# Performance work log

Measured on AMD Instinct MI355X. Metric: run time of the kernel, lower is better.

## Reference

```python
import jax, jax.numpy as jnp
import numpy as np

TEMP = 0.1
COEFF = 0.5
WARMUP = 0
S = 32 * 32  # hardcoded in the torch module


def _l2n(x, axis):
    # matches F.normalize(p=2, eps=1e-12)
    n = jnp.linalg.norm(x, axis=axis, keepdims=True)
    return x / jnp.maximum(n, 1e-12)


def _ce_first_class(pos, neg):
    # cross-entropy with label 0 on logits = [pos | neg] / T
    logits = jnp.concatenate([pos, neg], axis=1) / TEMP
    return jnp.mean(jax.nn.logsumexp(logits, axis=1) - logits[:, 0])


def _dense_losses(q_of, q_x, k_of, k_x, k_avg_dense):
    # q_of,k_of: (B,d,S) normalized; q_x,k_x: (B,C,S) normalized; k_avg_dense: (B,C) UN-normalized (torch bug preserved)
    B, C, _ = q_x.shape
    sim = jnp.einsum('bds,bdt->bst', q_of, k_of)          # (B,S,S)
    ind = jnp.argmax(sim, axis=2)                          # (B,S)
    idxg = jnp.take_along_axis(k_x, jnp.broadcast_to(ind[:, None, :], k_x.shape), axis=2)
    idxg = jax.lax.stop_gradient(idxg)                     # computed under torch.no_grad
    l_pos = jnp.sum(q_x * idxg, axis=1).reshape(-1, 1)     # (B*S,1)
    qf = jnp.transpose(q_x, (0, 2, 1)).reshape(-1, C)      # (B*S,C)
    l_neg_full = qf @ k_avg_dense.T                        # (B*S,B)
    # static mask: row n excludes column n // S
    base = np.stack([np.delete(np.arange(B), i) for i in range(B)])  # (B,B-1)
    neg_cols = jnp.asarray(np.repeat(base, S, axis=0))     # (B*S,B-1)
    l_neg = jnp.take_along_axis(l_neg_full, neg_cols, axis=1)
    return l_pos, l_neg


def _forward(original_features_q, avgpooled_global_q, x_q, avgpooled_dense_q,
             original_features_k, avgpooled_global_k, x_k, avgpooled_dense_k, epoch):
    of = jnp.concatenate([original_features_q, original_features_k], axis=0)
    ag = jnp.concatenate([avgpooled_global_q, avgpooled_global_k], axis=0)
    x = jnp.concatenate([x_q, x_k], axis=0)
    ad = jnp.concatenate([avgpooled_dense_q, avgpooled_dense_k], axis=0)

    # global InfoNCE
    agn = _l2n(ag, 1)
    sim = agn @ agn.T                                      # (2B,2B)
    n2 = sim.shape[0]
    B = n2 // 2
    rows = np.arange(n2)
    pos_cols = (rows + B) % n2
    pos = sim[jnp.asarray(rows), jnp.asarray(pos_cols)][:, None]
    neg_cols = np.stack([np.setdiff1d(rows, [i, pos_cols[i]]) for i in range(n2)])  # (2B,2B-2)
    neg = jnp.take_along_axis(sim, jnp.asarray(neg_cols), axis=1)
    global_loss = _ce_first_class(pos, neg)

    # dense InfoNCE
    b, d, h, w = of.shape
    of = _l2n(of.reshape(b, d, h * w), 1)
    xn = _l2n(x, 1)
    q_of, k_of = of[:b // 2], of[b // 2:]
    q_x, k_x = xn[:b // 2], xn[b // 2:]
    q_ad, k_ad = ad[:b // 2], ad[b // 2:]  # NOTE: un-normalized, matching the torch code
    p1, n1 = _dense_losses(q_of, q_x, k_of, k_x, k_ad)
    p2, n2_ = _dense_losses(k_of, k_x, q_of, q_x, q_ad)
    dense_loss = _ce_first_class(jnp.concatenate([p1, p2], axis=0),
                                 jnp.concatenate([n1, n2_], axis=0))

    if epoch > WARMUP:
        return COEFF * global_loss + (1.0 - COEFF) * dense_loss
    return global_loss


def setup_inputs() -> dict:
    key = jax.random.key(0)
    ks = jax.random.split(key, 8)
    B, d, C, h, w = 64, 256, 128, 32, 32
    return {
        'original_features_q': jax.random.normal(ks[0], (B, d, h, w), jnp.float32),
        'avgpooled_global_q': jax.random.normal(ks[1], (B, C), jnp.float32),
        'x_q': jax.random.normal(ks[2], (B, C, h * w), jnp.float32),
        'avgpooled_dense_q': jax.random.normal(ks[3], (B, C), jnp.float32),
        'original_features_k': jax.random.normal(ks[4], (B, d, h, w), jnp.float32),
        'avgpooled_global_k': jax.random.normal(ks[5], (B, C), jnp.float32),
        'x_k': jax.random.normal(ks[6], (B, C, h * w), jnp.float32),
        'avgpooled_dense_k': jax.random.normal(ks[7], (B, C), jnp.float32),
        'epoch': 5,
    }


def reference(original_features_q, avgpooled_global_q, x_q, avgpooled_dense_q,
              original_features_k, avgpooled_global_k, x_k, avgpooled_dense_k, epoch):
    return _forward(original_features_q, avgpooled_global_q, x_q, avgpooled_dense_q,
                    original_features_k, avgpooled_global_k, x_k, avgpooled_dense_k, epoch)
```

## Files before the change

### kernel.cpp

```cpp
#include <hip/hip_runtime.h>
#include <math.h>

#define TEMP_INV 10.0f

typedef unsigned long long u64;
typedef __attribute__((ext_vector_type(8))) __bf16 bf16x8;
typedef __attribute__((ext_vector_type(4))) float f32x4;

__device__ inline unsigned fkey(float v) {
  unsigned u = __float_as_uint(v);
  return (u & 0x80000000u) ? ~u : (u | 0x80000000u);
}

__device__ __forceinline__ void async_copy16(const void* gp, void* lp) {
  __builtin_amdgcn_global_load_lds(
      (__attribute__((address_space(1))) void*)(unsigned long long)gp,
      (__attribute__((address_space(3))) void*)(unsigned long long)lp,
      16, 0, 0);
}

__global__ __launch_bounds__(256) void kpre(
    const float* __restrict__ ofq, const float* __restrict__ ofk,
    __bf16* __restrict__ ofT, float* __restrict__ of_invn,
    const float* __restrict__ xq, const float* __restrict__ xk,
    float* __restrict__ x_invn,
    const float* __restrict__ adq, const float* __restrict__ adk,
    float* __restrict__ adt,
    const float* __restrict__ agq, const float* __restrict__ agk,
    float* __restrict__ gsum) {
  unsigned bx = blockIdx.x;
  int t = threadIdx.x;
  if (bx < 4096) {
    int s0 = (bx & 31) * 32, b = bx >> 5;
    const float* src = (b < 64) ? (ofq + (size_t)b * 262144) : (ofk + (size_t)(b - 64) * 262144);
    __shared__ __bf16 T[32][36];
    __shared__ float R[8][32];
    int dd = t >> 5, ss = t & 31;
    int wr = t >> 3, wd = t & 7;
    float ssq = 0.f;
    __bf16* out = ofT + (size_t)b * 262144 + (size_t)s0 * 256;
    for (int d0 = 0; d0 < 256; d0 += 32) {
      float v[4];
#pragma unroll
      for (int it = 0; it < 4; ++it) {
        int d = d0 + dd + 8 * it;
        v[it] = src[(size_t)d * 1024 + s0 + ss];
        ssq += v[it] * v[it];
      }
      __syncthreads();
#pragma unroll
      for (int it = 0; it < 4; ++it) T[ss][dd + 8 * it] = (__bf16)v[it];
      __syncthreads();
      *(uint2*)(out + (size_t)wr * 256 + d0 + wd * 4) = *(const uint2*)(&T[wr][wd * 4]);
    }
    R[dd][ss] = ssq;
    __syncthreads();
    if (t < 32) {
      float a = 0.f;
#pragma unroll
      for (int r = 0; r < 8; ++r) a += R[r][t];
      of_invn[b * 1024 + s0 + t] = 1.0f / fmaxf(sqrtf(a), 1e-12f);
    }
  } else if (bx < 4672) {
    unsigned px = bx - 4096;
    if (px < 512) {
      int idx = px * 256 + t;
      int b = idx >> 10, s = idx & 1023;
      const float* src = (b < 64) ? (xq + (size_t)b * 131072) : (xk + (size_t)(b - 64) * 131072);
      float acc = 0.f;
#pragma unroll 8
      for (int c = 0; c < 128; ++c) { float v = src[c * 1024 + s]; acc += v * v; }
      x_invn[idx] = 1.0f / fmaxf(sqrtf(acc), 1e-12f);
    } else {
      int i = (px - 512) * 256 + t;
      int dir = i >> 13, r = i & 8191;
      int j = r >> 7, c = r & 127;
      const float* ad = dir == 0 ? adk : adq;
      adt[dir * 8192 + c * 64 + j] = ad[j * 128 + c];
    }
  } else {
    __shared__ float logits[2][128];
    __shared__ float rinv[128];
    int ii = t >> 7, j = t & 127;
    int i = (int)(bx - 4672) * 2 + ii;
    const float* rowi = (i < 64) ? (agq + i * 128) : (agk + (i - 64) * 128);
    const float* rowj = (j < 64) ? (agq + j * 128) : (agk + (j - 64) * 128);
    float dot = 0.f, nj = 0.f;
#pragma unroll 8
    for (int c = 0; c < 128; ++c) { float a = rowi[c], bb = rowj[c]; dot += a * bb; nj += bb * bb; }
    if (ii == 0) rinv[j] = 1.0f / fmaxf(sqrtf(nj), 1e-12f);
    __syncthreads();
    logits[ii][j] = dot * rinv[i] * rinv[j] * TEMP_INV;
    __syncthreads();
    if (j == 0) {
      int pos = (i + 64) & 127;
      float m = -INFINITY;
      for (int tt = 0; tt < 128; ++tt) if (tt != i) m = fmaxf(m, logits[ii][tt]);
      float e = 0.f;
      for (int tt = 0; tt < 128; ++tt) if (tt != i) e += __expf(logits[ii][tt] - m);
      atomicAdd(gsum, m + __logf(e) - logits[ii][pos]);
    }
  }
}

__global__ __launch_bounds__(512, 2) void ksim(
    const __bf16* __restrict__ ofT, const float* __restrict__ of_invn,
    u64* __restrict__ best_row, u64* __restrict__ best_col) {
  unsigned h = blockIdx.x + (blockIdx.y << 2) + (blockIdx.z << 4);
  int xcd = h & 7;
  unsigned slot = h >> 3;
  int b = xcd + 8 * (int)(slot >> 4);
  int tile = slot & 15;
  int s0 = (tile & 3) * 256, t0 = (tile >> 2) * 256;

  const __bf16* Ag = ofT + (size_t)b * 262144;
  const __bf16* Bg = ofT + (size_t)(b + 64) * 262144;
  __shared__ __bf16 As[2][16384];
  __shared__ __bf16 Bs[2][16384];

  int t = threadIdx.x;
  int lane = t & 63, w = t >> 6;
  int lc = lane & 15, q = lane >> 4;
  int wm = w >> 2, wn = w & 3;

  f32x4 acc[8][4];
#pragma unroll
  for (int i = 0; i < 8; ++i)
#pragma unroll
    for (int j = 0; j < 4; ++j) acc[i][j] = (f32x4)(0.f);

  int aoff[8], boff[4];
#pragma unroll
  for (int i = 0; i < 8; ++i) {
    int mr = wm * 128 + i * 16 + lc;
    aoff[i] = mr * 64 + ((q ^ (mr & 7)) << 3);
  }
#pragma unroll
  for (int j = 0; j < 4; ++j) {
    int nc = wn * 64 + j * 16 + lc;
    boff[j] = nc * 64 + ((q ^ (nc & 7)) << 3);
  }

  int ms = t >> 3, gphys = t & 7;
  int lg = gphys ^ (ms & 7);
  size_t aSrc = (size_t)(s0 + ms) * 256 + lg * 8;
  size_t bSrc = (size_t)(t0 + ms) * 256 + lg * 8;

  auto STAGE = [&](int bufn, int k0) {
    char* aL = (char*)&As[bufn][0] + t * 16;
    char* bL = (char*)&Bs[bufn][0] + t * 16;
#pragma unroll
    for (int c = 0; c < 4; ++c) {
      async_copy16(Ag + aSrc + (size_t)c * 16384 + k0, aL + c * 8192);
      async_copy16(Bg + bSrc + (size_t)c * 16384 + k0, bL + c * 8192);
    }
  };

  STAGE(0, 0);
  __syncthreads();

  for (int it = 0; it < 4; ++it) {
    int buf = it & 1;
    if (it < 3) STAGE(buf ^ 1, (it + 1) * 64);
#pragma unroll
    for (int kk = 0; kk < 2; ++kk) {
      int kx = kk << 5;
      bf16x8 af[8], bfr[4];
#pragma unroll
      for (int i = 0; i < 8; ++i) af[i] = *(const bf16x8*)(&As[buf][0] + (aoff[i] ^ kx));
#pragma unroll
      for (int j = 0; j < 4; ++j) bfr[j] = *(const bf16x8*)(&Bs[buf][0] + (boff[j] ^ kx));
      __builtin_amdgcn_s_setprio(1);
#pragma unroll
      for (int i = 0; i < 8; ++i)
#pragma unroll
        for (int j = 0; j < 4; ++j)
          acc[i][j] = __builtin_amdgcn_mfma_f32_16x16x32_bf16(af[i], bfr[j], acc[i][j], 0, 0, 0);
      __builtin_amdgcn_s_setprio(0);
    }
    __syncthreads();
  }

  float sk[4];
#pragma unroll
  for (int j = 0; j < 4; ++j) sk[j] = of_invn[65536 + b * 1024 + t0 + wn * 64 + j * 16 + lc];
  float sq[32];
#pragma unroll
  for (int i = 0; i < 8; ++i)
#pragma unroll
    for (int e = 0; e < 4; ++e)
      sq[i * 4 + e] = of_invn[b * 1024 + s0 + wm * 128 + i * 16 + q * 4 + e];

  u64* browb = best_row + (size_t)b * 1024 + s0;
  u64* bcolb = best_col + (size_t)b * 1024 + t0;

#pragma unroll
  for (int i = 0; i < 8; ++i) {
#pragma unroll
    for (int e = 0; e < 4; ++e) {
      float v[4];
#pragma unroll
      for (int j = 0; j < 4; ++j) v[j] = acc[i][j][e] * sk[j];
      float vb = fmaxf(fmaxf(v[0], v[1]), fmaxf(v[2], v[3]));
#pragma unroll
      for (int mask = 1; mask <= 8; mask <<= 1) vb = fmaxf(vb, __shfl_xor(vb, mask));
      unsigned ib = 0xFFFFFFFFu;
#pragma unroll
      for (int j = 0; j < 4; ++j) {
        unsigned cand = (v[j] == vb) ? (unsigned)(t0 + wn * 64 + j * 16 + lc) : 0xFFFFFFFFu;
        ib = min(ib, cand);
      }
#pragma unroll
      for (int mask = 1; mask <= 8; mask <<= 1) ib = min(ib, __shfl_xor(ib, mask));
      if (lc == 0)
        atomicMax(browb + wm * 128 + i * 16 + q * 4 + e,
                  ((u64)fkey(vb) << 32) | (u64)(0xFFFFFFFFu - ib));
    }
  }

#pragma unroll
  for (int j = 0; j < 4; ++j) {
    float cb = -INFINITY;
#pragma unroll
    for (int i = 0; i < 8; ++i)
#pragma unroll
      for (int e = 0; e < 4; ++e) cb = fmaxf(cb, acc[i][j][e] * sq[i * 4 + e]);
    cb = fmaxf(cb, __shfl_xor(cb, 16));
    cb = fmaxf(cb, __shfl_xor(cb, 32));
    unsigned ib = 0xFFFFFFFFu;
#pragma unroll
    for (int i = 0; i < 8; ++i)
#pragma unroll
      for (int e = 0; e < 4; ++e) {
        float m2 = acc[i][j][e] * sq[i * 4 + e];
        unsigned cand = (m2 == cb) ? (unsigned)(s0 + wm * 128 + i * 16 + q * 4 + e) : 0xFFFFFFFFu;
        ib = min(ib, cand);
      }
    ib = min(ib, __shfl_xor(ib, 16));
    ib = min(ib, __shfl_xor(ib, 32));
    if (lane < 16)
      atomicMax(bcolb + wn * 64 + j * 16 + lane,
                ((u64)fkey(cb) << 32) | (u64)(0xFFFFFFFFu - ib));
  }
}

__global__ __launch_bounds__(512) void kpos(
    const float* __restrict__ xq, const float* __restrict__ xk,
    const float* __restrict__ x_invn,
    const u64* __restrict__ best_row, const u64* __restrict__ best_col,
    float* __restrict__ posl) {
  int b = blockIdx.x, dir = blockIdx.y, half = blockIdx.z;
  const float* xsrc = dir == 0 ? xq : xk;
  const float* xdst = dir == 0 ? xk : xq;
  const float* inv_src = x_invn + (dir ? 65536 : 0);
  const float* inv_dst = x_invn + (dir ? 0 : 65536);
  const u64* best = dir == 0 ? best_row : best_col;

  __shared__ float xrow[8][1024];
  __shared__ float sdinv[1024];
  int t = threadIdx.x;
  int s = half * 512 + t;
  sdinv[t] = inv_dst[b * 1024 + t];
  sdinv[t + 512] = inv_dst[b * 1024 + t + 512];
  u64 p = best[(size_t)b * 1024 + s];
  int sidx = (int)(0xFFFFFFFFu - (unsigned)(p & 0xFFFFFFFFull));
  const float* xsb = xsrc + (size_t)b * 131072;
  const float* xdb = xdst + (size_t)b * 131072;
  float acc = 0.f;
  for (int c0 = 0; c0 < 128; c0 += 8) {
    __syncthreads();
#pragma unroll
    for (int qq = 0; qq < 4; ++qq)
      ((float4*)xrow)[t + 512 * qq] = ((const float4*)(xdb + (size_t)c0 * 1024))[t + 512 * qq];
    __syncthreads();
#pragma unroll
    for (int cc = 0; cc < 8; ++cc)
      acc += xsb[(size_t)(c0 + cc) * 1024 + s] * xrow[cc][sidx];
  }
  posl[dir * 65536 + b * 1024 + s] = acc * inv_src[b * 1024 + s] * sdinv[sidx] * TEMP_INV;
}

__global__ __launch_bounds__(256) void kneg(
    const float* __restrict__ xq, const float* __restrict__ xk,
    const float* __restrict__ x_invn,
    const float* __restrict__ adt, const float* __restrict__ posl,
    float* __restrict__ dsum) {
  int st = blockIdx.x, b = blockIdx.y, dir = blockIdx.z;
  const float* xsrc = dir == 0 ? xq : xk;
  const float* inv_src = x_invn + (dir ? 65536 : 0);
  const float* Bt = adt + dir * 8192;

  __shared__ float red[16];

  int tid = threadIdx.x;
  int tx = tid & 15, ty = tid >> 4;
  int s0 = st * 64;
  const float* xb = xsrc + (size_t)b * 131072;

  float4 sinv4 = *reinterpret_cast<const float4*>(inv_src + b * 1024 + s0 + ty * 4);

  float acc[4][4];
#pragma unroll
  for (int i = 0; i < 4; ++i)
#pragma unroll
    for (int j = 0; j < 4; ++j) acc[i][j] = 0.f;

  const float* arow = xb + s0 + ty * 4;
  const float* brow = Bt + tx * 4;

#pragma unroll 4
  for (int kk = 0; kk < 128; ++kk) {
    float4 av = *reinterpret_cast<const float4*>(arow + (size_t)kk * 1024);
    float4 bv = *reinterpret_cast<const float4*>(brow + (size_t)kk * 64);
    float a[4] = {av.x * sinv4.x, av.y * sinv4.y, av.z * sinv4.z, av.w * sinv4.w};
    float bb[4] = {bv.x, bv.y, bv.z, bv.w};
#pragma unroll
    for (int i = 0; i < 4; ++i)
#pragma unroll
      for (int j = 0; j < 4; ++j) acc[i][j] += a[i] * bb[j];
  }

  float lsum = 0.f;
#pragma unroll
  for (int i = 0; i < 4; ++i) {
    int s = s0 + ty * 4 + i;
    float pos = posl[dir * 65536 + b * 1024 + s];
    float lg[4];
    float mloc = -INFINITY;
#pragma unroll
    for (int j = 0; j < 4; ++j) {
      int jg = tx * 4 + j;
      lg[j] = (jg == b) ? -INFINITY : acc[i][j] * TEMP_INV;
      mloc = fmaxf(mloc, lg[j]);
    }
#pragma unroll
    for (int mask = 1; mask <= 8; mask <<= 1) mloc = fmaxf(mloc, __shfl_xor(mloc, mask));
    float m = fmaxf(mloc, pos);
    float e = 0.f;
#pragma unroll
    for (int j = 0; j < 4; ++j) e += __expf(lg[j] - m);
#pragma unroll
    for (int mask = 1; mask <= 8; mask <<= 1) e += __shfl_xor(e, mask);
    if (tx == 0) lsum += m + __logf(e + __expf(pos - m)) - pos;
  }
  if (tx == 0) red[ty] = lsum;
  __syncthreads();
  if (tid == 0) {
    float v = 0.f;
#pragma unroll
    for (int r = 0; r < 16; ++r) v += red[r];
    atomicAdd(dsum, v);
  }
}

__global__ void kfinal(const float* __restrict__ gsum, const float* __restrict__ dsum,
                       const int* __restrict__ epoch, float* __restrict__ out) {
  if (threadIdx.x == 0) {
    float g = gsum[0] / 128.0f;
    float dn = dsum[0] / 131072.0f;
    out[0] = (epoch[0] > 0) ? (0.5f * g + 0.5f * dn) : g;
  }
}

extern "C" void kernel_launch(void* const* d_in, const int* in_sizes, int n_in,
                              void* d_out, int out_size, void* d_ws, size_t ws_size,
                              hipStream_t stream) {
  const float* ofq = (const float*)d_in[0];
  const float* agq = (const float*)d_in[1];
  const float* xq  = (const float*)d_in[2];
  const float* adq = (const float*)d_in[3];
  const float* ofk = (const float*)d_in[4];
  const float* agk = (const float*)d_in[5];
  const float* xk  = (const float*)d_in[6];
  const float* adk = (const float*)d_in[7];
  const int* epoch = (const int*)d_in[8];
  float* out = (float*)d_out;

  char* wsb = (char*)d_ws;
  __bf16* ofT = (__bf16*)wsb;
  u64* best_row = (u64*)(wsb + 67108864);
  u64* best_col = best_row + 65536;
  float* gsum = (float*)(best_col + 65536);
  float* dsum = gsum + 1;
  float* posl = dsum + 1;
  float* x_invn  = posl + 131072;
  float* of_invn = x_invn + 131072;
  float* adt = of_invn + 131072;

  hipMemsetAsync(best_row, 0, 65536ull * 8 * 2 + 8, stream);

  kpre<<<4736, 256, 0, stream>>>(ofq, ofk, ofT, of_invn, xq, xk, x_invn,
                                 adq, adk, adt, agq, agk, gsum);

  dim3 gs(4, 4, 64);
  ksim<<<gs, 512, 0, stream>>>(ofT, of_invn, best_row, best_col);

  dim3 gp(64, 2, 2);
  kpos<<<gp, 512, 0, stream>>>(xq, xk, x_invn, best_row, best_col, posl);

  dim3 gn(16, 64, 2);
  kneg<<<gn, 256, 0, stream>>>(xq, xk, x_invn, adt, posl, dsum);

  kfinal<<<1, 1, 0, stream>>>(gsum, dsum, epoch, out);
}
```

Baseline: 416.6 us.

## Batch transpose loads in kpre, merge kpos halves, stage kneg tiles in LDS

In kpre, all 32 loads per thread are issued up front and the per-chunk syncs are removed. This raises memory-level parallelism at the cost of more registers and a larger LDS buffer. kpos now uses 1024-thread blocks so each destination row tile is loaded once per batch rather than once per half. kneg stages the normalized A tile and the whole B matrix in shared memory so the GEMM inner loop reads from LDS instead of global memory, which adds LDS traffic and barriers.

```diff
diff --git a/kernel.cpp b/kernel.cpp
--- a/kernel.cpp
+++ b/kernel.cpp
@@ -33,28 +33,31 @@
   if (bx < 4096) {
     int s0 = (bx & 31) * 32, b = bx >> 5;
     const float* src = (b < 64) ? (ofq + (size_t)b * 262144) : (ofk + (size_t)(b - 64) * 262144);
-    __shared__ __bf16 T[32][36];
+    __shared__ __bf16 T[8][32][36];
     __shared__ float R[8][32];
     int dd = t >> 5, ss = t & 31;
     int wr = t >> 3, wd = t & 7;
+    float v[8][4];
+#pragma unroll
+    for (int d0i = 0; d0i < 8; ++d0i)
+#pragma unroll
+      for (int it = 0; it < 4; ++it)
+        v[d0i][it] = src[(size_t)(d0i * 32 + dd + 8 * it) * 1024 + s0 + ss];
     float ssq = 0.f;
+#pragma unroll
+    for (int d0i = 0; d0i < 8; ++d0i)
+#pragma unroll
+      for (int it = 0; it < 4; ++it) ssq += v[d0i][it] * v[d0i][it];
+#pragma unroll
+    for (int d0i = 0; d0i < 8; ++d0i)
+#pragma unroll
+      for (int it = 0; it < 4; ++it) T[d0i][ss][dd + 8 * it] = (__bf16)v[d0i][it];
+    R[dd][ss] = ssq;
+    __syncthreads();
     __bf16* out = ofT + (size_t)b * 262144 + (size_t)s0 * 256;
-    for (int d0 = 0; d0 < 256; d0 += 32) {
-      float v[4];
-#pragma unroll
-      for (int it = 0; it < 4; ++it) {
-        int d = d0 + dd + 8 * it;
-        v[it] = src[(size_t)d * 1024 + s0 + ss];
-        ssq += v[it] * v[it];
-      }
-      __syncthreads();
-#pragma unroll
-      for (int it = 0; it < 4; ++it) T[ss][dd + 8 * it] = (__bf16)v[it];
-      __syncthreads();
-      *(uint2*)(out + (size_t)wr * 256 + d0 + wd * 4) = *(const uint2*)(&T[wr][wd * 4]);
-    }
-    R[dd][ss] = ssq;
-    __syncthreads();
+#pragma unroll
+    for (int d0i = 0; d0i < 8; ++d0i)
+      *(uint2*)(out + (size_t)wr * 256 + d0i * 32 + wd * 4) = *(const uint2*)(&T[d0i][wr][wd * 4]);
     if (t < 32) {
       float a = 0.f;
 #pragma unroll
@@ -244,12 +247,12 @@
   }
 }
 
-__global__ __launch_bounds__(512) void kpos(
+__global__ __launch_bounds__(1024) void kpos(
     const float* __restrict__ xq, const float* __restrict__ xk,
     const float* __restrict__ x_invn,
     const u64* __restrict__ best_row, const u64* __restrict__ best_col,
     float* __restrict__ posl) {
-  int b = blockIdx.x, dir = blockIdx.y, half = blockIdx.z;
+  int b = blockIdx.x, dir = blockIdx.y;
   const float* xsrc = dir == 0 ? xq : xk;
   const float* xdst = dir == 0 ? xk : xq;
   const float* inv_src = x_invn + (dir ? 65536 : 0);
@@ -259,10 +262,8 @@
   __shared__ float xrow[8][1024];
   __shared__ float sdinv[1024];
   int t = threadIdx.x;
-  int s = half * 512 + t;
   sdinv[t] = inv_dst[b * 1024 + t];
-  sdinv[t + 512] = inv_dst[b * 1024 + t + 512];
-  u64 p = best[(size_t)b * 1024 + s];
+  u64 p = best[(size_t)b * 1024 + t];
   int sidx = (int)(0xFFFFFFFFu - (unsigned)(p & 0xFFFFFFFFull));
   const float* xsb = xsrc + (size_t)b * 131072;
   const float* xdb = xdst + (size_t)b * 131072;
@@ -270,14 +271,14 @@
   for (int c0 = 0; c0 < 128; c0 += 8) {
     __syncthreads();
 #pragma unroll
-    for (int qq = 0; qq < 4; ++qq)
-      ((float4*)xrow)[t + 512 * qq] = ((const float4*)(xdb + (size_t)c0 * 1024))[t + 512 * qq];
+    for (int qq = 0; qq < 2; ++qq)
+      ((float4*)xrow)[t + 1024 * qq] = ((const float4*)(xdb + (size_t)c0 * 1024))[t + 1024 * qq];
     __syncthreads();
 #pragma unroll
     for (int cc = 0; cc < 8; ++cc)
-      acc += xsb[(size_t)(c0 + cc) * 1024 + s] * xrow[cc][sidx];
-  }
-  posl[dir * 65536 + b * 1024 + s] = acc * inv_src[b * 1024 + s] * sdinv[sidx] * TEMP_INV;
+      acc += xsb[(size_t)(c0 + cc) * 1024 + t] * xrow[cc][sidx];
+  }
+  posl[dir * 65536 + b * 1024 + t] = acc * inv_src[b * 1024 + t] * sdinv[sidx] * TEMP_INV;
 }
 
 __global__ __launch_bounds__(256) void kneg(
@@ -290,34 +291,48 @@
   const float* inv_src = x_invn + (dir ? 65536 : 0);
   const float* Bt = adt + dir * 8192;
 
+  __shared__ float As2[64][64];
+  __shared__ float Bs2[128][64];
   __shared__ float red[16];
 
   int tid = threadIdx.x;
   int tx = tid & 15, ty = tid >> 4;
   int s0 = st * 64;
+
+#pragma unroll
+  for (int qq = 0; qq < 8; ++qq)
+    reinterpret_cast<float4*>(Bs2)[tid + 256 * qq] =
+        reinterpret_cast<const float4*>(Bt)[tid + 256 * qq];
+
+  float acc[4][4];
+#pragma unroll
+  for (int i = 0; i < 4; ++i)
+#pragma unroll
+    for (int j = 0; j < 4; ++j) acc[i][j] = 0.f;
+
+  int lm = tid & 63, lk = tid >> 6;
+  float sinv = inv_src[b * 1024 + s0 + lm];
   const float* xb = xsrc + (size_t)b * 131072;
 
-  float4 sinv4 = *reinterpret_cast<const float4*>(inv_src + b * 1024 + s0 + ty * 4);
-
-  float acc[4][4];
-#pragma unroll
-  for (int i = 0; i < 4; ++i)
-#pragma unroll
-    for (int j = 0; j < 4; ++j) acc[i][j] = 0.f;
-
-  const float* arow = xb + s0 + ty * 4;
-  const float* brow = Bt + tx * 4;
-
-#pragma unroll 4
-  for (int kk = 0; kk < 128; ++kk) {
-    float4 av = *reinterpret_cast<const float4*>(arow + (size_t)kk * 1024);
-    float4 bv = *reinterpret_cast<const float4*>(brow + (size_t)kk * 64);
-    float a[4] = {av.x * sinv4.x, av.y * sinv4.y, av.z * sinv4.z, av.w * sinv4.w};
-    float bb[4] = {bv.x, bv.y, bv.z, bv.w};
-#pragma unroll
-    for (int i = 0; i < 4; ++i)
-#pragma unroll
-      for (int j = 0; j < 4; ++j) acc[i][j] += a[i] * bb[j];
+  for (int k0 = 0; k0 < 128; k0 += 64) {
+#pragma unroll
+    for (int r = 0; r < 16; ++r) {
+      int kk = lk + 4 * r;
+      As2[kk][lm] = xb[(k0 + kk) * 1024 + s0 + lm] * sinv;
+    }
+    __syncthreads();
+#pragma unroll
+    for (int kk = 0; kk < 64; ++kk) {
+      float4 av = *reinterpret_cast<const float4*>(&As2[kk][ty * 4]);
+      float4 bv = *reinterpret_cast<const float4*>(&Bs2[k0 + kk][tx * 4]);
+      float a[4] = {av.x, av.y, av.z, av.w};
+      float bb[4] = {bv.x, bv.y, bv.z, bv.w};
+#pragma unroll
+      for (int i = 0; i < 4; ++i)
+#pragma unroll
+        for (int j = 0; j < 4; ++j) acc[i][j] += a[i] * bb[j];
+    }
+    __syncthreads();
   }
 
   float lsum = 0.f;
@@ -395,8 +410,8 @@
   dim3 gs(4, 4, 64);
   ksim<<<gs, 512, 0, stream>>>(ofT, of_invn, best_row, best_col);
 
-  dim3 gp(64, 2, 2);
-  kpos<<<gp, 512, 0, stream>>>(xq, xk, x_invn, best_row, best_col, posl);
+  dim3 gp(64, 2);
+  kpos<<<gp, 1024, 0, stream>>>(xq, xk, x_invn, best_row, best_col, posl);
 
   dim3 gn(16, 64, 2);
   kneg<<<gn, 256, 0, stream>>>(xq, xk, x_invn, adt, posl, dsum);
```

Result: faster. 385.5 us (-7.5%).
